# Kernel tuning notes

Hardware: AMD Instinct MI355X
Metric: run time of the kernel (lower is better)

The kernel has to match this reference:

```python
import jax, jax.numpy as jnp
import numpy as np

N, E, IN, H, C = 50000, 800000, 128, 4, 32


def setup_inputs() -> dict:
    key = jax.random.key(0)
    ks = jax.random.split(key, 10)
    scale = 1.0 / np.sqrt(IN)
    x = jax.random.normal(ks[0], (N, IN), dtype=jnp.float32)
    edge_index = jax.random.randint(ks[1], (2, E), 0, N, dtype=jnp.int64)
    Wq = jax.random.uniform(ks[2], (IN, H * C), jnp.float32, -scale, scale)
    bq = jnp.zeros((H * C,), jnp.float32)
    Wk = jax.random.uniform(ks[3], (IN, H * C), jnp.float32, -scale, scale)
    bk = jnp.zeros((H * C,), jnp.float32)
    Wv = jax.random.uniform(ks[4], (IN, H * C), jnp.float32, -scale, scale)
    bv = jnp.zeros((H * C,), jnp.float32)
    Wskip = jax.random.uniform(ks[5], (IN, H * C), jnp.float32, -scale, scale)
    bskip = jnp.zeros((H * C,), jnp.float32)
    return {"x": x, "edge_index": edge_index, "Wq": Wq, "bq": bq,
            "Wk": Wk, "bk": bk, "Wv": Wv, "bv": bv,
            "Wskip": Wskip, "bskip": bskip}


def reference(x, edge_index, Wq, bq, Wk, bk, Wv, bv, Wskip, bskip):
    # PyG TransformerConv: edge messages flow src -> dst
    src, dst = edge_index[0], edge_index[1]
    q = (x @ Wq + bq).reshape(N, H, C)
    k = (x @ Wk + bk).reshape(N, H, C)
    v = (x @ Wv + bv).reshape(N, H, C)
    # per-edge attention logits [E, H]
    alpha = jnp.einsum('ehc,ehc->eh', q[dst], k[src]) / jnp.sqrt(jnp.float32(C))
    # scatter-softmax over incoming edges of each dst node
    m = jax.ops.segment_max(alpha, dst, num_segments=N)  # [N, H]
    ex = jnp.exp(alpha - m[dst])
    denom = jax.ops.segment_sum(ex, dst, num_segments=N)  # [N, H]
    w = ex / denom[dst]  # [E, H]
    # weighted scatter-add of values
    agg = jax.ops.segment_sum(v[src] * w[:, :, None], dst, num_segments=N)  # [N,H,C]
    out = agg.reshape(N, H * C) + x @ Wskip + bskip
    return out
```

## Files before the change

kernel.cpp:

```cpp
#include <hip/hip_runtime.h>
#include <hip/hip_bf16.h>

#define NNODES 50000
#define NEDGES 800000
#define FDIM   128
#define NHEADS 4
#define NSCANB ((NNODES + 1023) / 1024)
#define NBLK   782
#define NT16   (NBLK * 4)
#define NFULL  3125

typedef __attribute__((ext_vector_type(8))) short  bf16x8;
typedef __attribute__((ext_vector_type(4))) float  f32x4;

static __device__ __forceinline__ unsigned short f2bf(float f) {
    __hip_bfloat16 h = __float2bfloat16(f);
    return *reinterpret_cast<unsigned short*>(&h);
}
static __device__ __forceinline__ float bf2f(unsigned short u) {
    return __uint_as_float(((unsigned int)u) << 16);
}

__global__ __launch_bounds__(256) void tgd_cvt_xa(const float* __restrict__ x,
                                                  unsigned short* __restrict__ xa)
{
    __shared__ unsigned short lds[16 * 136];
    const int gt  = blockIdx.x;
    const int tid = threadIdx.x;

    if (gt < NFULL) {
        const float* src = x + (size_t)gt * 2048 + tid * 8;
        float4 f0 = *reinterpret_cast<const float4*>(src);
        float4 f1 = *reinterpret_cast<const float4*>(src + 4);
        const int row = tid >> 4;
        const int col = (tid & 15) * 8;
        unsigned short* d = &lds[row * 136 + col];
        d[0]=f2bf(f0.x); d[1]=f2bf(f0.y); d[2]=f2bf(f0.z); d[3]=f2bf(f0.w);
        d[4]=f2bf(f1.x); d[5]=f2bf(f1.y); d[6]=f2bf(f1.z); d[7]=f2bf(f1.w);
    }
    __syncthreads();

    const int lane = tid & 63;
    const int ks   = tid >> 6;
    const int row  = lane & 15;
    const int k0   = ks * 32 + (lane >> 4) * 8;
    unsigned short u[8];
    if (gt < NFULL) {
        #pragma unroll
        for (int j = 0; j < 8; ++j) u[j] = lds[row * 136 + k0 + j];
    } else {
        #pragma unroll
        for (int j = 0; j < 8; ++j) u[j] = 0;
    }
    *reinterpret_cast<uint4*>(&xa[((size_t)gt * 256 + tid) * 8]) =
        *reinterpret_cast<uint4*>(u);
}

__global__ __launch_bounds__(256) void tgd_cvt_w(
    const float* __restrict__ Wq, const float* __restrict__ Wk,
    const float* __restrict__ Wv, const float* __restrict__ Wsk,
    unsigned short* __restrict__ Wt2)
{
    int t = blockIdx.x * 256 + threadIdx.x;
    if (t >= 4 * 8 * 4 * 64) return;
    int m    = t >> 11;
    int ct   = (t >> 8) & 7;
    int ks   = (t >> 6) & 3;
    int lane = t & 63;
    int c  = ct * 16 + (lane & 15);
    int k0 = ks * 32 + (lane >> 4) * 8;
    const float* W = (m == 0) ? Wq : (m == 1) ? Wk : (m == 2) ? Wv : Wsk;
    unsigned short u[8];
    #pragma unroll
    for (int j = 0; j < 8; ++j)
        u[j] = f2bf(W[(size_t)(k0 + j) * FDIM + c]);
    *reinterpret_cast<uint4*>(&Wt2[(size_t)t * 8]) = *reinterpret_cast<uint4*>(u);
}

__global__ __launch_bounds__(512) void tgd_gemm_mfma(
    const unsigned short* __restrict__ xa, const unsigned short* __restrict__ Wt2,
    const float* __restrict__ bq, const float* __restrict__ bk,
    const float* __restrict__ bv, const float* __restrict__ bsk,
    unsigned short* __restrict__ qb, unsigned short* __restrict__ kv,
    float* __restrict__ outp)
{
    __shared__ float st[64 * 128];
    unsigned short* sth = (unsigned short*)st;

    const int tid  = threadIdx.x;
    const int wave = tid >> 6, lane = tid & 63;
    const int mp   = wave >> 2;
    const int wr   = wave & 3;
    const int l16  = lane & 15, lhi = lane >> 4;
    const int gt   = blockIdx.x * 4 + wr;
    const int base = blockIdx.x * 64;

    bf16x8 a[4];
    #pragma unroll
    for (int ks = 0; ks < 4; ++ks)
        a[ks] = *reinterpret_cast<const bf16x8*>(
            xa + ((size_t)(gt * 4 + ks) * 64 + lane) * 8);

    f32x4 acc[2][8];
    #pragma unroll
    for (int m2 = 0; m2 < 2; ++m2)
        #pragma unroll
        for (int ct = 0; ct < 8; ++ct)
            acc[m2][ct] = (f32x4){0.f, 0.f, 0.f, 0.f};

    #pragma unroll
    for (int ks = 0; ks < 4; ++ks) {
        #pragma unroll
        for (int m2 = 0; m2 < 2; ++m2) {
            const int m = mp * 2 + m2;
            const unsigned short* wb =
                Wt2 + ((size_t)((m * 8 * 4 + ks) * 64) + lane) * 8;
            #pragma unroll
            for (int ct = 0; ct < 8; ++ct) {
                bf16x8 b = *reinterpret_cast<const bf16x8*>(wb + (size_t)ct * 2048);
                acc[m2][ct] = __builtin_amdgcn_mfma_f32_16x16x32_bf16(
                    a[ks], b, acc[m2][ct], 0, 0, 0);
            }
        }
    }

    const int rowl0 = wr * 16 + lhi * 4;

    if (mp == 0) {
        #pragma unroll
        for (int ct = 0; ct < 8; ++ct) {
            int col = ct * 16 + l16;
            float bval = bq[col];
            #pragma unroll
            for (int r = 0; r < 4; ++r)
                sth[(rowl0 + r) * 128 + col] = f2bf(acc[0][ct][r] + bval);
        }
    }
    __syncthreads();
    #pragma unroll
    for (int i = 0; i < 2; ++i) {
        int idx = i * 512 + tid;
        int row = idx >> 4, c8 = idx & 15;
        if (base + row < NNODES)
            *reinterpret_cast<uint4*>(&qb[(size_t)(base + row) * 128 + c8 * 8]) =
                *reinterpret_cast<const uint4*>(&sth[row * 128 + c8 * 8]);
    }
    __syncthreads();

    if (mp == 1) {
        #pragma unroll
        for (int ct = 0; ct < 8; ++ct) {
            int col = ct * 16 + l16;
            float bval = bsk[col];
            #pragma unroll
            for (int r = 0; r < 4; ++r)
                st[(rowl0 + r) * 128 + col] = acc[1][ct][r] + bval;
        }
    }
    __syncthreads();
    #pragma unroll
    for (int i = 0; i < 4; ++i) {
        int idx = i * 512 + tid;
        int row = idx >> 5, c4 = idx & 31;
        if (base + row < NNODES)
            *reinterpret_cast<float4*>(&outp[(size_t)(base + row) * FDIM + c4 * 4]) =
                *reinterpret_cast<const float4*>(&st[row * 128 + c4 * 4]);
    }
    __syncthreads();

    {
        const int off  = (mp == 0) ? 0 : 128;
        const int m2s  = (mp == 0) ? 1 : 0;
        const float* bias = (mp == 0) ? bk : bv;
        #pragma unroll
        for (int ct = 0; ct < 8; ++ct) {
            int col = ct * 16 + l16;
            float bval = bias[col];
            #pragma unroll
            for (int r = 0; r < 4; ++r)
                sth[(rowl0 + r) * 256 + off + col] = f2bf(acc[m2s][ct][r] + bval);
        }
    }
    __syncthreads();
    #pragma unroll
    for (int i = 0; i < 4; ++i) {
        int idx = i * 512 + tid;
        int row = idx >> 5, c8 = idx & 31;
        if (base + row < NNODES)
            *reinterpret_cast<uint4*>(&kv[(size_t)(base + row) * 256 + c8 * 8]) =
                *reinterpret_cast<const uint4*>(&sth[row * 256 + c8 * 8]);
    }
}

__global__ __launch_bounds__(256) void tgd_hist(const int* __restrict__ ei,
                                                int* __restrict__ deg)
{
    int t = blockIdx.x * 256 + threadIdx.x;
    if (t < NEDGES) atomicAdd(&deg[ei[NEDGES + t]], 1);
}

__global__ __launch_bounds__(1024) void tgd_scan1(const int* __restrict__ deg,
                                                  int* __restrict__ rowptr,
                                                  int* __restrict__ bsum)
{
    __shared__ int buf[1024];
    const int tid = threadIdx.x;
    const int i   = blockIdx.x * 1024 + tid;
    int d = (i < NNODES) ? deg[i] : 0;
    buf[tid] = d;
    __syncthreads();
    #pragma unroll
    for (int off = 1; off < 1024; off <<= 1) {
        int t2 = (tid >= off) ? buf[tid - off] : 0;
        __syncthreads();
        buf[tid] += t2;
        __syncthreads();
    }
    if (i < NNODES) rowptr[i + 1] = buf[tid];
    if (tid == 1023) bsum[blockIdx.x] = buf[1023];
}

__global__ __launch_bounds__(64) void tgd_scan2(const int* __restrict__ bsum,
                                                int* __restrict__ boff)
{
    int lane = threadIdx.x;
    int v = (lane < NSCANB) ? bsum[lane] : 0;
    int own = v;
    #pragma unroll
    for (int off = 1; off < 64; off <<= 1) {
        int t = __shfl_up(v, off);
        if (lane >= off) v += t;
    }
    if (lane < NSCANB) boff[lane] = v - own;
}

__global__ __launch_bounds__(1024) void tgd_scan3(const int* __restrict__ deg,
                                                  const int* __restrict__ boff,
                                                  int* __restrict__ rowptr,
                                                  int* __restrict__ ofs)
{
    const int i = blockIdx.x * 1024 + threadIdx.x;
    if (i < NNODES) {
        int r = rowptr[i + 1] + boff[blockIdx.x];
        rowptr[i + 1] = r;
        ofs[i] = r - deg[i];
    }
    if (i == 0) rowptr[0] = 0;
}

__global__ __launch_bounds__(256) void tgd_build(const int* __restrict__ ei,
                                                 int* __restrict__ ofs,
                                                 int* __restrict__ csr)
{
    int t = blockIdx.x * 256 + threadIdx.x;
    if (t >= NEDGES) return;
    int src = ei[t];
    int dst = ei[NEDGES + t];
    int pos = atomicAdd(&ofs[dst], 1);
    csr[pos] = src;
}

__global__ __launch_bounds__(256) void tgd_agg(
    const int* __restrict__ csr, const int* __restrict__ rowptr,
    const unsigned short* __restrict__ qb, const unsigned short* __restrict__ kv,
    float* __restrict__ outp)
{
    const int node = blockIdx.x * 4 + (threadIdx.x >> 6);
    const int lane = threadIdx.x & 63;
    if (node >= NNODES) return;
    const int start = rowptr[node];
    const int end   = rowptr[node + 1];
    if (start == end) return;

    const bool isK = (lane < 32);
    float4 qv = {0.f, 0.f, 0.f, 0.f};
    if (isK) {
        ushort4 qu = *reinterpret_cast<const ushort4*>(&qb[(size_t)node * FDIM + lane * 4]);
        qv.x = bf2f(qu.x); qv.y = bf2f(qu.y); qv.z = bf2f(qu.z); qv.w = bf2f(qu.w);
    }
    const float inv = 0.17677669529663687f;

    float  den = 0.0f;
    float4 acc = {0.f, 0.f, 0.f, 0.f};

    for (int base = start; base < end; base += 64) {
        const int cnt = min(64, end - base);
        int myid = (lane < cnt) ? csr[base + lane] : 0;

        int j = 0;
        for (; j + 3 < cnt; j += 4) {
            int s0 = __shfl(myid, j);
            int s1 = __shfl(myid, j + 1);
            int s2 = __shfl(myid, j + 2);
            int s3 = __shfl(myid, j + 3);
            ushort4 r0 = *reinterpret_cast<const ushort4*>(&kv[(size_t)s0 * 256 + lane * 4]);
            ushort4 r1 = *reinterpret_cast<const ushort4*>(&kv[(size_t)s1 * 256 + lane * 4]);
            ushort4 r2 = *reinterpret_cast<const ushort4*>(&kv[(size_t)s2 * 256 + lane * 4]);
            ushort4 r3 = *reinterpret_cast<const ushort4*>(&kv[(size_t)s3 * 256 + lane * 4]);

            float a0 = bf2f(r0.x), a1 = bf2f(r0.y), a2 = bf2f(r0.z), a3 = bf2f(r0.w);
            float b0 = bf2f(r1.x), b1 = bf2f(r1.y), b2 = bf2f(r1.z), b3 = bf2f(r1.w);
            float c0 = bf2f(r2.x), c1 = bf2f(r2.y), c2 = bf2f(r2.z), c3 = bf2f(r2.w);
            float d0 = bf2f(r3.x), d1 = bf2f(r3.y), d2 = bf2f(r3.z), d3 = bf2f(r3.w);

            float sA = qv.x*a0 + qv.y*a1 + qv.z*a2 + qv.w*a3;
            float sB = qv.x*b0 + qv.y*b1 + qv.z*b2 + qv.w*b3;
            float sC = qv.x*c0 + qv.y*c1 + qv.z*c2 + qv.w*c3;
            float sD = qv.x*d0 + qv.y*d1 + qv.z*d2 + qv.w*d3;
            sA += __shfl_xor(sA, 1);  sB += __shfl_xor(sB, 1);
            sC += __shfl_xor(sC, 1);  sD += __shfl_xor(sD, 1);
            sA += __shfl_xor(sA, 2);  sB += __shfl_xor(sB, 2);
            sC += __shfl_xor(sC, 2);  sD += __shfl_xor(sD, 2);
            sA += __shfl_xor(sA, 4);  sB += __shfl_xor(sB, 4);
            sC += __shfl_xor(sC, 4);  sD += __shfl_xor(sD, 4);
            float wA = __expf(sA * inv);
            float wB = __expf(sB * inv);
            float wC = __expf(sC * inv);
            float wD = __expf(sD * inv);
            wA = __shfl_xor(wA, 32);
            wB = __shfl_xor(wB, 32);
            wC = __shfl_xor(wC, 32);
            wD = __shfl_xor(wD, 32);
            if (!isK) {
                den += (wA + wB) + (wC + wD);
                acc.x += wA*a0 + wB*b0 + wC*c0 + wD*d0;
                acc.y += wA*a1 + wB*b1 + wC*c1 + wD*d1;
                acc.z += wA*a2 + wB*b2 + wC*c2 + wD*d2;
                acc.w += wA*a3 + wB*b3 + wC*c3 + wD*d3;
            }
        }
        for (; j + 1 < cnt; j += 2) {
            int s0 = __shfl(myid, j);
            int s1 = __shfl(myid, j + 1);
            ushort4 r0 = *reinterpret_cast<const ushort4*>(&kv[(size_t)s0 * 256 + lane * 4]);
            ushort4 r1 = *reinterpret_cast<const ushort4*>(&kv[(size_t)s1 * 256 + lane * 4]);
            float a0 = bf2f(r0.x), a1 = bf2f(r0.y), a2 = bf2f(r0.z), a3 = bf2f(r0.w);
            float b0 = bf2f(r1.x), b1 = bf2f(r1.y), b2 = bf2f(r1.z), b3 = bf2f(r1.w);
            float sA = qv.x*a0 + qv.y*a1 + qv.z*a2 + qv.w*a3;
            float sB = qv.x*b0 + qv.y*b1 + qv.z*b2 + qv.w*b3;
            sA += __shfl_xor(sA, 1);  sB += __shfl_xor(sB, 1);
            sA += __shfl_xor(sA, 2);  sB += __shfl_xor(sB, 2);
            sA += __shfl_xor(sA, 4);  sB += __shfl_xor(sB, 4);
            float wA = __expf(sA * inv);
            float wB = __expf(sB * inv);
            wA = __shfl_xor(wA, 32);
            wB = __shfl_xor(wB, 32);
            if (!isK) {
                den += wA + wB;
                acc.x += wA*a0 + wB*b0;
                acc.y += wA*a1 + wB*b1;
                acc.z += wA*a2 + wB*b2;
                acc.w += wA*a3 + wB*b3;
            }
        }
        if (j < cnt) {
            int s0 = __shfl(myid, j);
            ushort4 r0 = *reinterpret_cast<const ushort4*>(&kv[(size_t)s0 * 256 + lane * 4]);
            float a0 = bf2f(r0.x), a1 = bf2f(r0.y), a2 = bf2f(r0.z), a3 = bf2f(r0.w);
            float sA = qv.x*a0 + qv.y*a1 + qv.z*a2 + qv.w*a3;
            sA += __shfl_xor(sA, 1);
            sA += __shfl_xor(sA, 2);
            sA += __shfl_xor(sA, 4);
            float wA = __expf(sA * inv);
            wA = __shfl_xor(wA, 32);
            if (!isK) {
                den += wA;
                acc.x += wA*a0; acc.y += wA*a1; acc.z += wA*a2; acc.w += wA*a3;
            }
        }
    }

    if (!isK) {
        float invd = 1.0f / den;
        float4* o = reinterpret_cast<float4*>(&outp[(size_t)node * FDIM + (lane - 32) * 4]);
        float4 cur = *o;
        cur.x += acc.x * invd;
        cur.y += acc.y * invd;
        cur.z += acc.z * invd;
        cur.w += acc.w * invd;
        *o = cur;
    }
}

extern "C" void kernel_launch(void* const* d_in, const int* in_sizes, int n_in,
                              void* d_out, int out_size, void* d_ws, size_t ws_size,
                              hipStream_t stream) {
    const float* x   = (const float*)d_in[0];
    const int*   ei  = (const int*)  d_in[1];
    const float* Wq  = (const float*)d_in[2];
    const float* bq  = (const float*)d_in[3];
    const float* Wk  = (const float*)d_in[4];
    const float* bk  = (const float*)d_in[5];
    const float* Wv  = (const float*)d_in[6];
    const float* bv  = (const float*)d_in[7];
    const float* Wsk = (const float*)d_in[8];
    const float* bsk = (const float*)d_in[9];
    float* outp = (float*)d_out;

    unsigned short* qb  = (unsigned short*)d_ws;
    unsigned short* kv  = qb + (size_t)NNODES * FDIM;
    unsigned short* xa  = kv + (size_t)NNODES * 256;
    unsigned short* Wt2 = xa + (size_t)NT16 * 2048;
    int* deg    = (int*)(Wt2 + 4 * FDIM * FDIM);
    int* rowptr = deg + NNODES;
    int* ofs    = rowptr + NNODES + 1;
    int* csr    = ofs + NNODES;
    int* bsum   = csr + NEDGES;
    int* boff   = bsum + NSCANB;

    hipMemsetAsync(deg, 0, (size_t)NNODES * sizeof(int), stream);

    tgd_cvt_xa<<<NT16, 256, 0, stream>>>(x, xa);
    tgd_cvt_w<<<(4 * 8 * 4 * 64 + 255) / 256, 256, 0, stream>>>(Wq, Wk, Wv, Wsk, Wt2);

    tgd_gemm_mfma<<<NBLK, 512, 0, stream>>>(
        xa, Wt2, bq, bk, bv, bsk, qb, kv, outp);

    tgd_hist<<<(NEDGES + 255) / 256, 256, 0, stream>>>(ei, deg);
    tgd_scan1<<<NSCANB, 1024, 0, stream>>>(deg, rowptr, bsum);
    tgd_scan2<<<1, 64, 0, stream>>>(bsum, boff);
    tgd_scan3<<<NSCANB, 1024, 0, stream>>>(deg, boff, rowptr, ofs);
    tgd_build<<<(NEDGES + 255) / 256, 256, 0, stream>>>(ei, ofs, csr);
    tgd_agg<<<(NNODES + 3) / 4, 256, 0, stream>>>(csr, rowptr, qb, kv, outp);
}
```

Measured before the change: 296.3 us.

## Fuse x conversion, degree histogram and scans into fewer kernels

The separate x-to-bf16 conversion kernel is removed. The GEMM now loads fp32 x directly, converts it into LDS and reads A fragments from there. The degree zeroing moves into the weight-conversion kernel, replacing the memset, and the edge histogram atomics are appended to the GEMM kernel. The scan2 kernel is folded into scan3, where each block reduces the preceding block sums itself. Together these cut kernel launches and the intermediate xa buffer round-trip, at the cost of extra LDS traffic and syncs in the GEMM.

```diff
diff --git a/kernel.cpp b/kernel.cpp
--- a/kernel.cpp
+++ b/kernel.cpp
@@ -7,8 +7,6 @@
 #define NHEADS 4
 #define NSCANB ((NNODES + 1023) / 1024)
 #define NBLK   782
-#define NT16   (NBLK * 4)
-#define NFULL  3125
 
 typedef __attribute__((ext_vector_type(8))) short  bf16x8;
 typedef __attribute__((ext_vector_type(4))) float  f32x4;
@@ -21,66 +19,39 @@
     return __uint_as_float(((unsigned int)u) << 16);
 }
 
-__global__ __launch_bounds__(256) void tgd_cvt_xa(const float* __restrict__ x,
-                                                  unsigned short* __restrict__ xa)
-{
-    __shared__ unsigned short lds[16 * 136];
-    const int gt  = blockIdx.x;
-    const int tid = threadIdx.x;
-
-    if (gt < NFULL) {
-        const float* src = x + (size_t)gt * 2048 + tid * 8;
-        float4 f0 = *reinterpret_cast<const float4*>(src);
-        float4 f1 = *reinterpret_cast<const float4*>(src + 4);
-        const int row = tid >> 4;
-        const int col = (tid & 15) * 8;
-        unsigned short* d = &lds[row * 136 + col];
-        d[0]=f2bf(f0.x); d[1]=f2bf(f0.y); d[2]=f2bf(f0.z); d[3]=f2bf(f0.w);
-        d[4]=f2bf(f1.x); d[5]=f2bf(f1.y); d[6]=f2bf(f1.z); d[7]=f2bf(f1.w);
-    }
-    __syncthreads();
-
-    const int lane = tid & 63;
-    const int ks   = tid >> 6;
-    const int row  = lane & 15;
-    const int k0   = ks * 32 + (lane >> 4) * 8;
-    unsigned short u[8];
-    if (gt < NFULL) {
-        #pragma unroll
-        for (int j = 0; j < 8; ++j) u[j] = lds[row * 136 + k0 + j];
-    } else {
-        #pragma unroll
-        for (int j = 0; j < 8; ++j) u[j] = 0;
-    }
-    *reinterpret_cast<uint4*>(&xa[((size_t)gt * 256 + tid) * 8]) =
-        *reinterpret_cast<uint4*>(u);
-}
-
-__global__ __launch_bounds__(256) void tgd_cvt_w(
+__global__ __launch_bounds__(256) void tgd_prep(
     const float* __restrict__ Wq, const float* __restrict__ Wk,
     const float* __restrict__ Wv, const float* __restrict__ Wsk,
-    unsigned short* __restrict__ Wt2)
-{
-    int t = blockIdx.x * 256 + threadIdx.x;
-    if (t >= 4 * 8 * 4 * 64) return;
-    int m    = t >> 11;
-    int ct   = (t >> 8) & 7;
-    int ks   = (t >> 6) & 3;
-    int lane = t & 63;
-    int c  = ct * 16 + (lane & 15);
-    int k0 = ks * 32 + (lane >> 4) * 8;
-    const float* W = (m == 0) ? Wq : (m == 1) ? Wk : (m == 2) ? Wv : Wsk;
-    unsigned short u[8];
-    #pragma unroll
-    for (int j = 0; j < 8; ++j)
-        u[j] = f2bf(W[(size_t)(k0 + j) * FDIM + c]);
-    *reinterpret_cast<uint4*>(&Wt2[(size_t)t * 8]) = *reinterpret_cast<uint4*>(u);
+    unsigned short* __restrict__ Wt2, int* __restrict__ deg)
+{
+    const int b = blockIdx.x;
+    if (b < 32) {
+        int t = b * 256 + threadIdx.x;
+        int m    = t >> 11;
+        int ct   = (t >> 8) & 7;
+        int ks   = (t >> 6) & 3;
+        int lane = t & 63;
+        int c  = ct * 16 + (lane & 15);
+        int k0 = ks * 32 + (lane >> 4) * 8;
+        const float* W = (m == 0) ? Wq : (m == 1) ? Wk : (m == 2) ? Wv : Wsk;
+        unsigned short u[8];
+        #pragma unroll
+        for (int j = 0; j < 8; ++j)
+            u[j] = f2bf(W[(size_t)(k0 + j) * FDIM + c]);
+        *reinterpret_cast<uint4*>(&Wt2[(size_t)t * 8]) = *reinterpret_cast<uint4*>(u);
+    } else {
+        int i0 = ((b - 32) * 256 + threadIdx.x) * 4;
+        #pragma unroll
+        for (int j = 0; j < 4; ++j)
+            if (i0 + j < NNODES) deg[i0 + j] = 0;
+    }
 }
 
 __global__ __launch_bounds__(512) void tgd_gemm_mfma(
-    const unsigned short* __restrict__ xa, const unsigned short* __restrict__ Wt2,
+    const float* __restrict__ x, const unsigned short* __restrict__ Wt2,
     const float* __restrict__ bq, const float* __restrict__ bk,
     const float* __restrict__ bv, const float* __restrict__ bsk,
+    const int* __restrict__ ei, int* __restrict__ deg,
     unsigned short* __restrict__ qb, unsigned short* __restrict__ kv,
     float* __restrict__ outp)
 {
@@ -92,14 +63,28 @@
     const int mp   = wave >> 2;
     const int wr   = wave & 3;
     const int l16  = lane & 15, lhi = lane >> 4;
-    const int gt   = blockIdx.x * 4 + wr;
     const int base = blockIdx.x * 64;
+
+    #pragma unroll
+    for (int i = 0; i < 4; ++i) {
+        int f = i * 512 + tid;
+        int row = f >> 5, c4 = f & 31;
+        float4 v4 = {0.f, 0.f, 0.f, 0.f};
+        if (base + row < NNODES)
+            v4 = *reinterpret_cast<const float4*>(
+                &x[(size_t)(base + row) * FDIM + c4 * 4]);
+        unsigned short* d = &sth[row * 136 + c4 * 4];
+        d[0] = f2bf(v4.x); d[1] = f2bf(v4.y);
+        d[2] = f2bf(v4.z); d[3] = f2bf(v4.w);
+    }
+    __syncthreads();
 
     bf16x8 a[4];
     #pragma unroll
     for (int ks = 0; ks < 4; ++ks)
         a[ks] = *reinterpret_cast<const bf16x8*>(
-            xa + ((size_t)(gt * 4 + ks) * 64 + lane) * 8);
+            &sth[(wr * 16 + l16) * 136 + ks * 32 + lhi * 8]);
+    __syncthreads();
 
     f32x4 acc[2][8];
     #pragma unroll
@@ -190,13 +175,12 @@
             *reinterpret_cast<uint4*>(&kv[(size_t)(base + row) * 256 + c8 * 8]) =
                 *reinterpret_cast<const uint4*>(&sth[row * 256 + c8 * 8]);
     }
-}
-
-__global__ __launch_bounds__(256) void tgd_hist(const int* __restrict__ ei,
-                                                int* __restrict__ deg)
-{
-    int t = blockIdx.x * 256 + threadIdx.x;
-    if (t < NEDGES) atomicAdd(&deg[ei[NEDGES + t]], 1);
+
+    {
+        int e0 = blockIdx.x * 1024 + tid * 2;
+        if (e0 < NEDGES)     atomicAdd(&deg[ei[NEDGES + e0]], 1);
+        if (e0 + 1 < NEDGES) atomicAdd(&deg[ei[NEDGES + e0 + 1]], 1);
+    }
 }
 
 __global__ __launch_bounds__(1024) void tgd_scan1(const int* __restrict__ deg,
@@ -220,28 +204,23 @@
     if (tid == 1023) bsum[blockIdx.x] = buf[1023];
 }
 
-__global__ __launch_bounds__(64) void tgd_scan2(const int* __restrict__ bsum,
-                                                int* __restrict__ boff)
-{
-    int lane = threadIdx.x;
-    int v = (lane < NSCANB) ? bsum[lane] : 0;
-    int own = v;
-    #pragma unroll
-    for (int off = 1; off < 64; off <<= 1) {
-        int t = __shfl_up(v, off);
-        if (lane >= off) v += t;
-    }
-    if (lane < NSCANB) boff[lane] = v - own;
-}
-
 __global__ __launch_bounds__(1024) void tgd_scan3(const int* __restrict__ deg,
-                                                  const int* __restrict__ boff,
+                                                  const int* __restrict__ bsum,
                                                   int* __restrict__ rowptr,
                                                   int* __restrict__ ofs)
 {
-    const int i = blockIdx.x * 1024 + threadIdx.x;
+    __shared__ int sboff;
+    const int tid = threadIdx.x;
+    if (tid < 64) {
+        int v = (tid < blockIdx.x) ? bsum[tid] : 0;
+        #pragma unroll
+        for (int m = 32; m >= 1; m >>= 1) v += __shfl_xor(v, m);
+        if (tid == 0) sboff = v;
+    }
+    __syncthreads();
+    const int i = blockIdx.x * 1024 + tid;
     if (i < NNODES) {
-        int r = rowptr[i + 1] + boff[blockIdx.x];
+        int r = rowptr[i + 1] + sboff;
         rowptr[i + 1] = r;
         ofs[i] = r - deg[i];
     }
@@ -399,27 +378,21 @@
 
     unsigned short* qb  = (unsigned short*)d_ws;
     unsigned short* kv  = qb + (size_t)NNODES * FDIM;
-    unsigned short* xa  = kv + (size_t)NNODES * 256;
-    unsigned short* Wt2 = xa + (size_t)NT16 * 2048;
+    unsigned short* Wt2 = kv + (size_t)NNODES * 256;
     int* deg    = (int*)(Wt2 + 4 * FDIM * FDIM);
     int* rowptr = deg + NNODES;
     int* ofs    = rowptr + NNODES + 1;
     int* csr    = ofs + NNODES;
     int* bsum   = csr + NEDGES;
-    int* boff   = bsum + NSCANB;
-
-    hipMemsetAsync(deg, 0, (size_t)NNODES * sizeof(int), stream);
-
-    tgd_cvt_xa<<<NT16, 256, 0, stream>>>(x, xa);
-    tgd_cvt_w<<<(4 * 8 * 4 * 64 + 255) / 256, 256, 0, stream>>>(Wq, Wk, Wv, Wsk, Wt2);
+
+    tgd_prep<<<32 + NSCANB, 256, 0, stream>>>(Wq, Wk, Wv, Wsk, Wt2, deg);
 
     tgd_gemm_mfma<<<NBLK, 512, 0, stream>>>(
-        xa, Wt2, bq, bk, bv, bsk, qb, kv, outp);
-
-    tgd_hist<<<(NEDGES + 255) / 256, 256, 0, stream>>>(ei, deg);
+        x, Wt2, bq, bk, bv, bsk, ei, deg, qb, kv, outp);
+
     tgd_scan1<<<NSCANB, 1024, 0, stream>>>(deg, rowptr, bsum);
-    tgd_scan2<<<1, 64, 0, stream>>>(bsum, boff);
-    tgd_scan3<<<NSCANB, 1024, 0, stream>>>(deg, boff, rowptr, ofs);
+    tgd_scan3<<<NSCANB, 1024, 0, stream>>>(deg, bsum, rowptr, ofs);
     tgd_build<<<(NEDGES + 255) / 256, 256, 0, stream>>>(ei, ofs, csr);
+
     tgd_agg<<<(NNODES + 3) / 4, 256, 0, stream>>>(csr, rowptr, qb, kv, outp);
 }
```

After: 275.0 us. -7.2%, faster.
